# Kernel optimization log

Measured on AMD Instinct MI355X. Metric: run time of the kernel, lower is better.

The kernel has to match this reference:

```python
import jax, jax.numpy as jnp
import numpy as np

B, N, D = 8, 4096, 128
P, K = 256, 64            # n_patches, n_pts_per_patch (= FoldingNet num_fine)
DFF, GRID = 1024, 2
G2 = GRID * GRID
NC = K // G2              # num_coarse
EPS = 1e-5                # BatchNorm eps (eval mode, running stats)


def fps(xyz, n):
    """Farthest point sampling on one cloud xyz [N,3] -> n int32 indices."""
    Np = xyz.shape[0]
    def step(carry, _):
        mind, last = carry
        d = jnp.sum((xyz - xyz[last]) ** 2, -1)
        mind = jnp.minimum(mind, d)
        nxt = jnp.argmax(mind).astype(jnp.int32)
        return (mind, nxt), nxt
    (_, _), idx = jax.lax.scan(step, (jnp.full((Np,), 1e10, xyz.dtype), jnp.int32(0)), None, length=n - 1)
    return jnp.concatenate([jnp.zeros((1,), jnp.int32), idx])


def setup_inputs() -> dict:
    key = jax.random.key(0)
    ks = jax.random.split(key, 24)
    rn = lambda i, s, sc=1.0: sc * jax.random.normal(ks[i], s, dtype=jnp.float32)
    inp = {
        'xyz': rn(0, (B, N, 3)),
        'feat': rn(1, (B, N, D)),
        # FoldingNet.xyz_mlp (Linear weights stored [in,out])
        'w1': rn(2, (D, DFF), 0.09), 'b1': rn(3, (DFF,), 0.02),
        'w2': rn(4, (DFF, DFF), 0.03), 'b2': rn(5, (DFF,), 0.02),
        'w3': rn(6, (DFF, 3 * NC), 0.03), 'b3': rn(7, (3 * NC,), 0.02),
        # FoldingNet.final_conv (1x1 conv weights stored [in,out]), BN eval stats
        'cw1': rn(8, (D + 5, DFF), 0.09), 'cb1': rn(9, (DFF,), 0.02),
        'g1': 0.5 + jax.random.uniform(ks[10], (DFF,), dtype=jnp.float32),
        'be1': rn(11, (DFF,), 0.02), 'm1': rn(12, (DFF,), 0.1),
        'v1': 0.5 + jax.random.uniform(ks[13], (DFF,), dtype=jnp.float32),
        'cw2': rn(14, (DFF, DFF), 0.03), 'cb2': rn(15, (DFF,), 0.02),
        'g2': 0.5 + jax.random.uniform(ks[16], (DFF,), dtype=jnp.float32),
        'be2': rn(17, (DFF,), 0.02), 'm2': rn(18, (DFF,), 0.1),
        'v2': 0.5 + jax.random.uniform(ks[19], (DFF,), dtype=jnp.float32),
        'cw3': rn(20, (DFF, 3), 0.03), 'cb3': rn(21, (3,), 0.02),
    }
    return inp


def reference(xyz, feat, w1, b1, w2, b2, w3, b3,
              cw1, cb1, g1, be1, m1, v1,
              cw2, cb2, g2, be2, m2, v2, cw3, cb3):
    # ---- point_forward: FPS -> square_distance -> masked topk -> gather -> maxpool ----
    fidx = jax.vmap(lambda p: fps(p, P))(xyz)                          # [B,P]
    patch_xyz = jnp.take_along_axis(xyz, fidx[:, :, None], 1)          # [B,P,3]
    d = (jnp.sum(xyz ** 2, -1)[:, :, None]
         + jnp.sum(patch_xyz ** 2, -1)[:, None, :]
         - 2.0 * jnp.einsum('bnc,bpc->bnp', xyz, patch_xyz))           # [B,N,P]
    # equal-sized dense batches => to_dense_batch mask is all-true (no 1e10 fill needed)
    _, gidx = jax.lax.top_k(-jnp.swapaxes(d, 1, 2), K)                 # [B,P,K] nearest
    bidx = jnp.arange(B)[:, None, None]
    grouped_feat = feat[bidx, gidx]                                    # [B,P,K,D]
    patch_feat = jnp.max(grouped_feat, axis=-2)                        # [B,P,D]
    grouped_xyz_norm = xyz[bidx, gidx] - patch_xyz[:, :, None, :]      # [B,P,K,3]

    # ---- FoldingNet decoder ----
    pf = patch_feat.reshape(B * P, D)
    h = jax.nn.relu(pf @ w1 + b1)
    h = jax.nn.relu(h @ w2 + b2)
    coarse = (h @ w3 + b3).reshape(B * P, NC, 3)                       # [BP,NC,3]
    pts = jnp.repeat(coarse, G2, axis=1)                               # [BP,K,3] (center)
    a = jnp.linspace(-0.05, 0.05, GRID, dtype=pf.dtype)
    seed2 = jnp.stack([jnp.tile(a, GRID), jnp.repeat(a, GRID)], -1)    # [G2,2]
    seedf = jnp.tile(seed2, (NC, 1))                                   # [K,2]
    featc = jnp.concatenate([
        jnp.broadcast_to(pf[:, None, :], (B * P, K, D)),
        jnp.broadcast_to(seedf[None], (B * P, K, 2)),
        pts], axis=-1)                                                 # [BP,K,D+5]
    bn = lambda x, g, be, m, v: (x - m) * (g * jax.lax.rsqrt(v + EPS)) + be
    h1 = jax.nn.relu(bn(featc @ cw1 + cb1, g1, be1, m1, v1))
    h2 = jax.nn.relu(bn(h1 @ cw2 + cb2, g2, be2, m2, v2))
    fine = h2 @ cw3 + cb3 + pts                                        # [BP,K,3]

    # ---- Chamfer L2 (mean(dist1)+mean(dist2)) between fine and grouped points ----
    gxyz = grouped_xyz_norm.reshape(B * P, K, 3)
    dd = jnp.sum((fine[:, :, None, :] - gxyz[:, None, :, :]) ** 2, -1) # [BP,K,K]
    loss_recon = jnp.mean(jnp.min(dd, axis=2)) + jnp.mean(jnp.min(dd, axis=1))
    return loss_recon
```

## Files before the change

kernel.cpp:

```cpp
#include <hip/hip_runtime.h>
#include <hip/hip_bf16.h>
#include <stdint.h>

#define DEV __device__ __forceinline__

using bf16x8  = __attribute__((ext_vector_type(8))) __bf16;
using floatx4 = __attribute__((ext_vector_type(4))) float;
using int32x8 = __attribute__((ext_vector_type(8))) int;

constexpr int Bb  = 8;
constexpr int Nn  = 4096;
constexpr int Dd  = 128;
constexpr int Pp  = 256;
constexpr int Kk  = 64;
constexpr int BP  = Bb * Pp;
constexpr int M2  = BP * Kk;
constexpr float EPSBN = 1e-5f;

DEV unsigned short f2bf(float f) {
  uint32_t u = __float_as_uint(f);
  u += 0x7fffu + ((u >> 16) & 1u);
  return (unsigned short)(u >> 16);
}
DEV float bf2f(unsigned short h) { return __uint_as_float(((uint32_t)h) << 16); }

DEV void async_copy16(const void* g, const void* l) {
  __builtin_amdgcn_global_load_lds(
      (__attribute__((address_space(1))) uint32_t*)(uintptr_t)g,
      (__attribute__((address_space(3))) uint32_t*)(uint32_t)(uintptr_t)l,
      16, 0, 0);
}

__global__ void prep_k(const float* g1, const float* be1, const float* m1, const float* v1, const float* cb1,
                       const float* g2, const float* be2, const float* m2, const float* v2, const float* cb2,
                       float* sc1, float* sh1, float* sc2, float* sh2, float* out) {
  int t = threadIdx.x;
  float s1 = g1[t] * rsqrtf(v1[t] + EPSBN);
  sc1[t] = s1; sh1[t] = (cb1[t] - m1[t]) * s1 + be1[t];
  float s2 = g2[t] * rsqrtf(v2[t] + EPSBN);
  sc2[t] = s2; sh2[t] = (cb2[t] - m2[t]) * s2 + be2[t];
  if (t == 0) out[0] = 0.f;
}

__global__ void cvt16(const float* __restrict__ in, unsigned short* __restrict__ out, int Kd, int Nd) {
  __shared__ float ts[32][33];
  int tx = threadIdx.x & 31, ty = threadIdx.x >> 5;
  int n0 = blockIdx.x * 32, k0 = blockIdx.y * 32;
#pragma unroll
  for (int r = 0; r < 4; ++r)
    ts[ty + 8 * r][tx] = in[(size_t)(k0 + ty + 8 * r) * Nd + n0 + tx];
  __syncthreads();
#pragma unroll
  for (int r = 0; r < 4; ++r)
    out[(size_t)(n0 + ty + 8 * r) * Kd + k0 + tx] = f2bf(ts[tx][ty + 8 * r]);
}

__global__ void cvt8(const float* __restrict__ in, uint8_t* __restrict__ out, int Kd, int Nd) {
  __shared__ float ts[32][33];
  int tx = threadIdx.x & 31, ty = threadIdx.x >> 5;
  int n0 = blockIdx.x * 32, k0 = blockIdx.y * 32;
#pragma unroll
  for (int r = 0; r < 4; ++r)
    ts[ty + 8 * r][tx] = in[(size_t)(k0 + ty + 8 * r) * Nd + n0 + tx];
  __syncthreads();
#pragma unroll
  for (int r = 0; r < 4; ++r) {
    float v = ts[tx][ty + 8 * r];
    int w = __builtin_amdgcn_cvt_pk_fp8_f32(v, v, 0, false);
    out[(size_t)(n0 + ty + 8 * r) * Kd + k0 + tx] = (uint8_t)(w & 0xff);
  }
}

#define DPPF(v, CTRL) __uint_as_float((uint32_t)__builtin_amdgcn_update_dpp( \
    (int)__float_as_uint(v), (int)__float_as_uint(v), CTRL, 0xF, 0xF, false))
#define DPPI(v, CTRL) __builtin_amdgcn_update_dpp(v, v, CTRL, 0xF, 0xF, false)
#define RSTEP2(CTRL) { \
    float od = DPPF(bv, CTRL); \
    int oi = DPPI(bi, CTRL); \
    bool tk = (od > bv) || (od == bv && oi < bi); \
    bv = tk ? od : bv; bi = tk ? oi : bi; }

__global__ __launch_bounds__(256)
void fps_k(const float* __restrict__ xyz, float* __restrict__ pxyz) {
  int b = blockIdx.x, tid = threadIdx.x;
  int lane = tid & 63, wv = tid >> 6;
  __shared__ float xs[Nn], ys[Nn], zs[Nn];
  __shared__ uint64_t cand[2][4];
  float xr[16], yr[16], zr[16], md[16];
#pragma unroll
  for (int j = 0; j < 16; ++j) {
    int i = tid + j * 256;
    const float* q = &xyz[(size_t)(b * Nn + i) * 3];
    float x = q[0], y = q[1], z = q[2];
    xr[j] = x; yr[j] = y; zr[j] = z; md[j] = 1e10f;
    xs[i] = x; ys[i] = y; zs[i] = z;
  }
  __syncthreads();
  const float* q0 = &xyz[(size_t)(b * Nn) * 3];
  float lx = q0[0], ly = q0[1], lz = q0[2];
  if (tid == 0) {
    pxyz[(size_t)(b * Pp) * 3 + 0] = lx;
    pxyz[(size_t)(b * Pp) * 3 + 1] = ly;
    pxyz[(size_t)(b * Pp) * 3 + 2] = lz;
  }
  for (int p = 1; p < Pp; ++p) {
    float bv = -1.f; int bi = 0x7fffffff;
#pragma unroll
    for (int j = 0; j < 16; ++j) {
      float dx = __fadd_rn(xr[j], -lx);
      float dy = __fadd_rn(yr[j], -ly);
      float dz = __fadd_rn(zr[j], -lz);
      float d = __fadd_rn(__fadd_rn(__fmul_rn(dx, dx), __fmul_rn(dy, dy)), __fmul_rn(dz, dz));
      float m = fminf(md[j], d);
      md[j] = m;
      if (m > bv) { bv = m; bi = tid + j * 256; }
    }
    RSTEP2(0x111) RSTEP2(0x112) RSTEP2(0x114) RSTEP2(0x118) RSTEP2(0x142) RSTEP2(0x143)
    int s = p & 1;
    if (lane == 63)
      cand[s][wv] = ((uint64_t)(uint32_t)__float_as_uint(bv) << 32) |
                    (uint32_t)(0x7fffffff - bi);
    __syncthreads();
    uint64_t k0 = cand[s][0], k1 = cand[s][1], k2 = cand[s][2], k3 = cand[s][3];
    uint64_t ka = (k0 > k1) ? k0 : k1;
    uint64_t kb = (k2 > k3) ? k2 : k3;
    uint64_t kw = (ka > kb) ? ka : kb;
    int wi = 0x7fffffff - (int)(uint32_t)(kw & 0xffffffffu);
    lx = xs[wi]; ly = ys[wi]; lz = zs[wi];
    if (tid == 0) {
      pxyz[(size_t)(b * Pp + p) * 3 + 0] = lx;
      pxyz[(size_t)(b * Pp + p) * 3 + 1] = ly;
      pxyz[(size_t)(b * Pp + p) * 3 + 2] = lz;
    }
  }
}

__global__ __launch_bounds__(256)
void group_k(const float* __restrict__ xyz, const float* __restrict__ feat,
             const float* __restrict__ pxyz, unsigned short* __restrict__ pfb,
             float* __restrict__ gxyz) {
  int bp = blockIdx.x, tid = threadIdx.x;
  int b = bp >> 8;
  __shared__ uint32_t dbits[Nn];
  __shared__ uint32_t hist[256];
  __shared__ int sel[64];
  __shared__ uint32_t svDigit, svWant, svClt, svCeq;
  __shared__ float red[256];
  float px = pxyz[(size_t)bp * 3], py = pxyz[(size_t)bp * 3 + 1], pz = pxyz[(size_t)bp * 3 + 2];
  for (int i = tid; i < Nn; i += 256) {
    const float* q = &xyz[(size_t)(b * Nn + i) * 3];
    float dx = q[0] - px, dy = q[1] - py, dz = q[2] - pz;
    dbits[i] = __float_as_uint(dx * dx + dy * dy + dz * dz);
  }
  uint32_t prefix = 0, want = 64;
  for (int shift = 24; shift >= 0; shift -= 8) {
    __syncthreads();
    hist[tid] = 0;
    __syncthreads();
    for (int i = tid; i < Nn; i += 256) {
      uint32_t v = dbits[i];
      bool match = (shift == 24) || ((v >> (shift + 8)) == prefix);
      if (match) atomicAdd(&hist[(v >> shift) & 255], 1u);
    }
    __syncthreads();
    uint32_t myh = hist[tid];
    for (int off = 1; off < 256; off <<= 1) {
      uint32_t o = (tid >= off) ? hist[tid - off] : 0u;
      __syncthreads();
      hist[tid] += o;
      __syncthreads();
    }
    uint32_t cum = hist[tid];
    uint32_t prev = cum - myh;
    if (prev < want && want <= cum) { svDigit = (uint32_t)tid; svWant = want - prev; }
    __syncthreads();
    prefix = (prefix << 8) | svDigit;
    want = svWant;
  }
  uint32_t tval = prefix;
  if (tid == 0) { svClt = 0; svCeq = 0; }
  __syncthreads();
  for (int i = tid; i < Nn; i += 256) {
    if (dbits[i] < tval) { uint32_t pos = atomicAdd(&svClt, 1u); sel[pos] = i; }
  }
  __syncthreads();
  uint32_t clt = svClt;
  for (int i = tid; i < Nn; i += 256) {
    if (dbits[i] == tval) {
      uint32_t pos = atomicAdd(&svCeq, 1u);
      if (clt + pos < 64) sel[clt + pos] = i;
    }
  }
  __syncthreads();
  if (tid < 192) {
    int k = tid / 3, c = tid - k * 3;
    float sub = (c == 0) ? px : (c == 1) ? py : pz;
    gxyz[(size_t)bp * 192 + tid] = xyz[(size_t)(b * Nn + sel[k]) * 3 + c] - sub;
  }
  int dch = tid & 127, half = tid >> 7;
  float m = -1e30f;
  for (int k = half * 32; k < half * 32 + 32; ++k)
    m = fmaxf(m, feat[(size_t)(b * Nn + sel[k]) * Dd + dch]);
  red[tid] = m;
  __syncthreads();
  if (half == 0) pfb[(size_t)bp * Dd + dch] = f2bf(fmaxf(m, red[tid + 128]));
}

template <int EPI>
__global__ __launch_bounds__(256)
void gemm_bt(const unsigned short* __restrict__ A, const unsigned short* __restrict__ Bt,
             float* __restrict__ Cf, unsigned short* __restrict__ Ch,
             const float* __restrict__ p0,
             int Npar, int Kd, int nbn) {
  __shared__ __align__(16) unsigned short As[128 * 32];
  __shared__ __align__(16) unsigned short Bs[128 * 32];
  const int tid = threadIdx.x;
  const int lane = tid & 63, wid = tid >> 6;
  const int bn = blockIdx.x % nbn, bm = blockIdx.x / nbn;
  const int m0 = bm * 128, n0 = bn * 128;
  const int quad = lane >> 4, l15 = lane & 15;
  const int wm = wid & 1, wn = wid >> 1;

  floatx4 acc[4][4];
#pragma unroll
  for (int i = 0; i < 4; ++i)
#pragma unroll
    for (int j = 0; j < 4; ++j) acc[i][j] = floatx4{0.f, 0.f, 0.f, 0.f};

  const int c0i = tid, c1i = tid + 256;
  const int r0 = c0i >> 2, o0 = (c0i & 3) * 8;
  const int r1 = c1i >> 2, o1 = (c1i & 3) * 8;

  for (int k0 = 0; k0 < Kd; k0 += 32) {
    async_copy16(A + (size_t)(m0 + r0) * Kd + k0 + o0, &As[c0i * 8]);
    async_copy16(A + (size_t)(m0 + r1) * Kd + k0 + o1, &As[c1i * 8]);
    async_copy16(Bt + (size_t)(n0 + r0) * Kd + k0 + o0, &Bs[c0i * 8]);
    async_copy16(Bt + (size_t)(n0 + r1) * Kd + k0 + o1, &Bs[c1i * 8]);
    __syncthreads();
    const bf16x8* Ap = reinterpret_cast<const bf16x8*>(As);
    const bf16x8* Bp = reinterpret_cast<const bf16x8*>(Bs);
    bf16x8 af[4], bfv[4];
#pragma unroll
    for (int t = 0; t < 4; ++t) {
      af[t]  = Ap[(wm * 64 + t * 16 + l15) * 4 + quad];
      bfv[t] = Bp[(wn * 64 + t * 16 + l15) * 4 + quad];
    }
#pragma unroll
    for (int mt = 0; mt < 4; ++mt)
#pragma unroll
      for (int nt = 0; nt < 4; ++nt)
        acc[mt][nt] = __builtin_amdgcn_mfma_f32_16x16x32_bf16(af[mt], bfv[nt], acc[mt][nt], 0, 0, 0);
    __syncthreads();
  }

  const int rowBase = m0 + wm * 64 + quad * 4;
  const int colBase = n0 + wn * 64 + l15;

  if (EPI == 0) {
#pragma unroll
    for (int mt = 0; mt < 4; ++mt)
#pragma unroll
      for (int nt = 0; nt < 4; ++nt)
#pragma unroll
        for (int r = 0; r < 4; ++r)
          Cf[(size_t)(rowBase + mt * 16 + r) * Npar + colBase + nt * 16] = acc[mt][nt][r];
  } else {
#pragma unroll
    for (int nt = 0; nt < 4; ++nt) {
      float bias = p0[colBase + nt * 16];
#pragma unroll
      for (int mt = 0; mt < 4; ++mt)
#pragma unroll
        for (int r = 0; r < 4; ++r) {
          float v = fmaxf(acc[mt][nt][r] + bias, 0.f);
          Ch[(size_t)(rowBase + mt * 16 + r) * Npar + colBase + nt * 16] = f2bf(v);
        }
    }
  }
}

__global__ __launch_bounds__(256)
void gemm_mx3(const float* __restrict__ u1, const float* __restrict__ cw1,
              const float* __restrict__ coarse, const float* __restrict__ sc1,
              const float* __restrict__ sh1,
              const uint8_t* __restrict__ Bt,
              const float* __restrict__ p0, const float* __restrict__ p1,
              const float* __restrict__ cw3, const float* __restrict__ cb3,
              float* __restrict__ fine) {
  __shared__ __align__(128) uint8_t As[32 * 1024];
  __shared__ __align__(128) uint8_t Bs[128 * 128];
  __shared__ float fsum[2][2][16][3];
  const int tid = threadIdx.x;
  const int lane = tid & 63, wid = tid >> 6;
  const int bm = blockIdx.x;
  const int quad = lane >> 4, l15 = lane & 15;
  const int wm = wid & 1, wn = wid >> 1;
  const int bp = bm >> 1;

  {
    int n0c = tid * 4;
    float4 un  = *(const float4*)&u1[(size_t)bp * 1024 + n0c];
    float4 a0  = *(const float4*)&cw1[128 * 1024 + n0c];
    float4 a1  = *(const float4*)&cw1[129 * 1024 + n0c];
    float4 b0  = *(const float4*)&cw1[130 * 1024 + n0c];
    float4 b1v = *(const float4*)&cw1[131 * 1024 + n0c];
    float4 b2v = *(const float4*)&cw1[132 * 1024 + n0c];
    float4 sc  = *(const float4*)&sc1[n0c];
    float4 sh  = *(const float4*)&sh1[n0c];
    const float sxv[4] = {-0.05f, 0.05f, -0.05f, 0.05f};
    const float syv[4] = {-0.05f, -0.05f, 0.05f, 0.05f};
    uint32_t* Aw = (uint32_t*)As;
    int gc = tid >> 2;
    int dw = tid & 3;
    for (int row = 0; row < 32; ++row) {
      int gi = row & 3;
      int j = (bm & 1) * 8 + (row >> 2);
      float c0 = coarse[(size_t)bp * 48 + j * 3 + 0];
      float c1 = coarse[(size_t)bp * 48 + j * 3 + 1];
      float c2 = coarse[(size_t)bp * 48 + j * 3 + 2];
      float sx = sxv[gi], sy = syv[gi];
      float x0 = un.x + sx * a0.x + sy * a1.x + c0 * b0.x + c1 * b1v.x + c2 * b2v.x;
      float x1 = un.y + sx * a0.y + sy * a1.y + c0 * b0.y + c1 * b1v.y + c2 * b2v.y;
      float x2 = un.z + sx * a0.z + sy * a1.z + c0 * b0.z + c1 * b1v.z + c2 * b2v.z;
      float x3 = un.w + sx * a0.w + sy * a1.w + c0 * b0.w + c1 * b1v.w + c2 * b2v.w;
      float v0 = fmaxf(x0 * sc.x + sh.x, 0.f);
      float v1 = fmaxf(x1 * sc.y + sh.y, 0.f);
      float v2 = fmaxf(x2 * sc.z + sh.z, 0.f);
      float v3 = fmaxf(x3 * sc.w + sh.w, 0.f);
      int w = __builtin_amdgcn_cvt_pk_fp8_f32(v0, v1, 0, false);
      w = __builtin_amdgcn_cvt_pk_fp8_f32(v2, v3, w, true);
      int phys = (gc & ~7) | ((gc & 7) ^ (row & 7));
      Aw[row * 256 + phys * 4 + dw] = (uint32_t)w;
    }
  }
  float fp[4][3];
#pragma unroll
  for (int r = 0; r < 4; ++r) fp[r][0] = fp[r][1] = fp[r][2] = 0.f;
  __syncthreads();

  const uint4* Ap = (const uint4*)As;
  const int rm = wm * 16 + l15;
  const int swm = rm & 7;

  for (int bn = 0; bn < 8; ++bn) {
    const int n0 = bn * 128;
    floatx4 acc[4];
#pragma unroll
    for (int j = 0; j < 4; ++j) acc[j] = floatx4{0.f, 0.f, 0.f, 0.f};

    for (int k0 = 0; k0 < 1024; k0 += 128) {
#pragma unroll
      for (int c = 0; c < 4; ++c) {
        int ci = c * 256 + tid;
        int row = ci >> 3, cp = ci & 7;
        int cc = cp ^ (row & 7);
        async_copy16(Bt + (size_t)(n0 + row) * 1024 + k0 + cc * 16, &Bs[ci * 16]);
      }
      __syncthreads();
      const uint4* Bp = (const uint4*)Bs;
      int kc = k0 >> 4;
      uint4 alo = Ap[rm * 64 + kc + ((2 * quad) ^ swm)];
      uint4 ahi = Ap[rm * 64 + kc + ((2 * quad + 1) ^ swm)];
      int32x8 av = int32x8{(int)alo.x, (int)alo.y, (int)alo.z, (int)alo.w,
                           (int)ahi.x, (int)ahi.y, (int)ahi.z, (int)ahi.w};
      int32x8 bv[4];
#pragma unroll
      for (int nt = 0; nt < 4; ++nt) {
        int rn = wn * 64 + nt * 16 + l15;
        int swn = rn & 7;
        uint4 blo = Bp[rn * 8 + ((2 * quad) ^ swn)];
        uint4 bhi = Bp[rn * 8 + ((2 * quad + 1) ^ swn)];
        bv[nt] = int32x8{(int)blo.x, (int)blo.y, (int)blo.z, (int)blo.w,
                         (int)bhi.x, (int)bhi.y, (int)bhi.z, (int)bhi.w};
      }
#pragma unroll
      for (int nt = 0; nt < 4; ++nt)
        acc[nt] = __builtin_amdgcn_mfma_scale_f32_16x16x128_f8f6f4(
            av, bv[nt], acc[nt], 0, 0, 0, 127, 0, 127);
      __syncthreads();
    }

#pragma unroll
    for (int nt = 0; nt < 4; ++nt) {
      int col = n0 + wn * 64 + nt * 16 + l15;
      float sc = p0[col], sh = p1[col];
      float c0 = cw3[col * 3], c1 = cw3[col * 3 + 1], c2 = cw3[col * 3 + 2];
#pragma unroll
      for (int r = 0; r < 4; ++r) {
        float v = fmaxf(acc[nt][r] * sc + sh, 0.f);
        fp[r][0] += v * c0; fp[r][1] += v * c1; fp[r][2] += v * c2;
      }
    }
  }

#pragma unroll
  for (int off = 1; off < 16; off <<= 1)
#pragma unroll
    for (int r = 0; r < 4; ++r)
#pragma unroll
      for (int i = 0; i < 3; ++i)
        fp[r][i] += __shfl_xor(fp[r][i], off, 64);
  if (l15 == 0) {
#pragma unroll
    for (int r = 0; r < 4; ++r)
#pragma unroll
      for (int i = 0; i < 3; ++i)
        fsum[wm][wn][quad * 4 + r][i] = fp[r][i];
  }
  __syncthreads();
  if (tid < 96) {
    int row = tid / 3, i = tid - row * 3;
    float s = fsum[row >> 4][0][row & 15][i] + fsum[row >> 4][1][row & 15][i];
    int g = bm * 32 + row;
    int j = (bm & 1) * 8 + ((row & 31) >> 2);
    fine[(size_t)g * 3 + i] = s + cb3[i] + coarse[(size_t)bp * 48 + j * 3 + i];
  }
}

__global__ __launch_bounds__(256)
void coarse_k(const unsigned short* __restrict__ h2m, const float* __restrict__ w3,
              const float* __restrict__ b3, float* __restrict__ coarse) {
  int r = blockIdx.x, tid = threadIdx.x;
  __shared__ float hrow[1024];
  __shared__ float part[192];
  for (int i = tid; i < 1024; i += 256) hrow[i] = bf2f(h2m[(size_t)r * 1024 + i]);
  __syncthreads();
  if (tid < 192) {
    int j = tid % 48, seg = tid / 48;
    float acc = 0.f;
    for (int k = seg * 256; k < seg * 256 + 256; ++k) acc += hrow[k] * w3[(size_t)k * 48 + j];
    part[tid] = acc;
  }
  __syncthreads();
  if (tid < 48)
    coarse[(size_t)r * 48 + tid] = part[tid] + part[tid + 48] + part[tid + 96] + part[tid + 144] + b3[tid];
}

__global__ __launch_bounds__(256)
void chamfer_k(const float* __restrict__ fine, const float* __restrict__ gxyz,
               float* __restrict__ out) {
  int tid = threadIdx.x, wv = tid >> 6, lane = tid & 63;
  int bp = blockIdx.x * 4 + wv;
  __shared__ float sf[4][64][3], sg[4][64][3];
  const float* fr = &fine[(size_t)(bp * 64 + lane) * 3];
  const float* gr = &gxyz[(size_t)(bp * 64 + lane) * 3];
  sf[wv][lane][0] = fr[0]; sf[wv][lane][1] = fr[1]; sf[wv][lane][2] = fr[2];
  sg[wv][lane][0] = gr[0]; sg[wv][lane][1] = gr[1]; sg[wv][lane][2] = gr[2];
  __syncthreads();
  float f0 = sf[wv][lane][0], f1 = sf[wv][lane][1], f2 = sf[wv][lane][2];
  float g0 = sg[wv][lane][0], g1 = sg[wv][lane][1], g2 = sg[wv][lane][2];
  float rmin = 1e30f, cmin = 1e30f;
  for (int j = 0; j < 64; ++j) {
    float dx = f0 - sg[wv][j][0], dy = f1 - sg[wv][j][1], dz = f2 - sg[wv][j][2];
    rmin = fminf(rmin, dx * dx + dy * dy + dz * dz);
    float ex = sf[wv][j][0] - g0, ey = sf[wv][j][1] - g1, ez = sf[wv][j][2] - g2;
    cmin = fminf(cmin, ex * ex + ey * ey + ez * ez);
  }
  float tot = rmin + cmin;
  for (int off = 32; off; off >>= 1) tot += __shfl_down(tot, off, 64);
  if (lane == 0) atomicAdd(out, tot * (1.0f / 131072.0f));
}

extern "C" void kernel_launch(void* const* d_in, const int* in_sizes, int n_in,
                              void* d_out, int out_size, void* d_ws, size_t ws_size,
                              hipStream_t stream) {
  (void)in_sizes; (void)n_in; (void)out_size; (void)ws_size;
  const float* xyz = (const float*)d_in[0];
  const float* feat = (const float*)d_in[1];
  const float* w1 = (const float*)d_in[2];
  const float* b1 = (const float*)d_in[3];
  const float* w2 = (const float*)d_in[4];
  const float* b2 = (const float*)d_in[5];
  const float* w3 = (const float*)d_in[6];
  const float* b3 = (const float*)d_in[7];
  const float* cw1 = (const float*)d_in[8];
  const float* cb1 = (const float*)d_in[9];
  const float* g1 = (const float*)d_in[10];
  const float* be1 = (const float*)d_in[11];
  const float* m1 = (const float*)d_in[12];
  const float* v1 = (const float*)d_in[13];
  const float* cw2 = (const float*)d_in[14];
  const float* cb2 = (const float*)d_in[15];
  const float* g2 = (const float*)d_in[16];
  const float* be2 = (const float*)d_in[17];
  const float* m2 = (const float*)d_in[18];
  const float* v2 = (const float*)d_in[19];
  const float* cw3 = (const float*)d_in[20];
  const float* cb3 = (const float*)d_in[21];
  float* out = (float*)d_out;

  uint8_t* ws = (uint8_t*)d_ws;
  size_t off = 0;
  auto alloc = [&](size_t bytes) {
    void* p = ws + off;
    off = (off + bytes + 255) & ~(size_t)255;
    return p;
  };
  float*          pxyz  = (float*)alloc((size_t)BP * 3 * 4);
  unsigned short* w1t   = (unsigned short*)alloc((size_t)1024 * 128 * 2);
  unsigned short* cw1t  = (unsigned short*)alloc((size_t)1024 * 128 * 2);
  unsigned short* w2t   = (unsigned short*)alloc((size_t)1024 * 1024 * 2);
  uint8_t*        cw2t8 = (uint8_t*)alloc((size_t)1024 * 1024);
  float*          sc1   = (float*)alloc(4096);
  float*          sh1   = (float*)alloc(4096);
  float*          sc2   = (float*)alloc(4096);
  float*          sh2   = (float*)alloc(4096);
  unsigned short* pfb   = (unsigned short*)alloc((size_t)BP * 128 * 2);
  float*          gxyz  = (float*)alloc((size_t)BP * 64 * 3 * 4);
  float*          u1    = (float*)alloc((size_t)BP * 1024 * 4);
  unsigned short* hb    = (unsigned short*)alloc((size_t)BP * 1024 * 2);
  unsigned short* h2m   = (unsigned short*)alloc((size_t)BP * 1024 * 2);
  float*          coarse = (float*)alloc((size_t)BP * 48 * 4);
  float*          fine  = (float*)alloc((size_t)M2 * 3 * 4);

  prep_k<<<1, 1024, 0, stream>>>(g1, be1, m1, v1, cb1, g2, be2, m2, v2, cb2,
                                 sc1, sh1, sc2, sh2, out);
  cvt16<<<dim3(1024 / 32, 128 / 32), 256, 0, stream>>>(w1, w1t, 128, 1024);
  cvt16<<<dim3(1024 / 32, 128 / 32), 256, 0, stream>>>(cw1, cw1t, 128, 1024);
  cvt16<<<dim3(1024 / 32, 1024 / 32), 256, 0, stream>>>(w2, w2t, 1024, 1024);
  cvt8<<<dim3(1024 / 32, 1024 / 32), 256, 0, stream>>>(cw2, cw2t8, 1024, 1024);
  fps_k<<<Bb, 256, 0, stream>>>(xyz, pxyz);
  group_k<<<BP, 256, 0, stream>>>(xyz, feat, pxyz, pfb, gxyz);
  gemm_bt<0><<<(2048 / 128) * 8, 256, 0, stream>>>(pfb, cw1t, u1, nullptr, nullptr,
                                                   1024, 128, 8);
  gemm_bt<1><<<(2048 / 128) * 8, 256, 0, stream>>>(pfb, w1t, nullptr, hb, b1,
                                                   1024, 128, 8);
  gemm_bt<1><<<(2048 / 128) * 8, 256, 0, stream>>>(hb, w2t, nullptr, h2m, b2,
                                                   1024, 1024, 8);
  coarse_k<<<2048, 256, 0, stream>>>(h2m, w3, b3, coarse);
  gemm_mx3<<<M2 / 32, 256, 0, stream>>>(u1, cw1, coarse, sc1, sh1,
                                        cw2t8, sc2, sh2, cw3, cb3, fine);
  chamfer_k<<<BP / 4, 256, 0, stream>>>(fine, gxyz, out);
}
```

Baseline: 691.0 us.

## Enlarge fused MX-FP8 GEMM tile to 128 rows with double-buffered B staging

```diff
diff --git a/kernel.cpp b/kernel.cpp
--- a/kernel.cpp
+++ b/kernel.cpp
@@ -279,7 +279,7 @@
   }
 }
 
-__global__ __launch_bounds__(256)
+__global__ __launch_bounds__(256, 1)
 void gemm_mx3(const float* __restrict__ u1, const float* __restrict__ cw1,
               const float* __restrict__ coarse, const float* __restrict__ sc1,
               const float* __restrict__ sh1,
@@ -287,19 +287,35 @@
               const float* __restrict__ p0, const float* __restrict__ p1,
               const float* __restrict__ cw3, const float* __restrict__ cb3,
               float* __restrict__ fine) {
-  __shared__ __align__(128) uint8_t As[32 * 1024];
-  __shared__ __align__(128) uint8_t Bs[128 * 128];
-  __shared__ float fsum[2][2][16][3];
+  __shared__ __align__(128) uint8_t As[128 * 1024];
+  __shared__ __align__(128) uint8_t Bs[2][128 * 128];
   const int tid = threadIdx.x;
   const int lane = tid & 63, wid = tid >> 6;
   const int bm = blockIdx.x;
   const int quad = lane >> 4, l15 = lane & 15;
   const int wm = wid & 1, wn = wid >> 1;
-  const int bp = bm >> 1;
+  const int bp0 = bm * 2;
+
+  auto stageB = [&](int it, uint8_t* buf) {
+    int n0 = (it >> 3) * 128, k0 = (it & 7) * 128;
+#pragma unroll
+    for (int c = 0; c < 4; ++c) {
+      int ci = c * 256 + tid;
+      int row = ci >> 3, cp = ci & 7;
+      int cc = cp ^ (row & 7);
+      async_copy16(Bt + (size_t)(n0 + row) * 1024 + k0 + cc * 16, &buf[ci * 16]);
+    }
+  };
+
+  stageB(0, Bs[0]);
+  float* coLds = (float*)Bs[1];
+  if (tid < 96) coLds[tid] = coarse[(size_t)bp0 * 48 + tid];
+  __syncthreads();
 
   {
     int n0c = tid * 4;
-    float4 un  = *(const float4*)&u1[(size_t)bp * 1024 + n0c];
+    float4 un0 = *(const float4*)&u1[(size_t)bp0 * 1024 + n0c];
+    float4 un1 = *(const float4*)&u1[(size_t)(bp0 + 1) * 1024 + n0c];
     float4 a0  = *(const float4*)&cw1[128 * 1024 + n0c];
     float4 a1  = *(const float4*)&cw1[129 * 1024 + n0c];
     float4 b0  = *(const float4*)&cw1[130 * 1024 + n0c];
@@ -310,19 +326,26 @@
     const float sxv[4] = {-0.05f, 0.05f, -0.05f, 0.05f};
     const float syv[4] = {-0.05f, -0.05f, 0.05f, 0.05f};
     uint32_t* Aw = (uint32_t*)As;
-    int gc = tid >> 2;
-    int dw = tid & 3;
-    for (int row = 0; row < 32; ++row) {
-      int gi = row & 3;
-      int j = (bm & 1) * 8 + (row >> 2);
-      float c0 = coarse[(size_t)bp * 48 + j * 3 + 0];
-      float c1 = coarse[(size_t)bp * 48 + j * 3 + 1];
-      float c2 = coarse[(size_t)bp * 48 + j * 3 + 2];
-      float sx = sxv[gi], sy = syv[gi];
-      float x0 = un.x + sx * a0.x + sy * a1.x + c0 * b0.x + c1 * b1v.x + c2 * b2v.x;
-      float x1 = un.y + sx * a0.y + sy * a1.y + c0 * b0.y + c1 * b1v.y + c2 * b2v.y;
-      float x2 = un.z + sx * a0.z + sy * a1.z + c0 * b0.z + c1 * b1v.z + c2 * b2v.z;
-      float x3 = un.w + sx * a0.w + sy * a1.w + c0 * b0.w + c1 * b1v.w + c2 * b2v.w;
+    int gc = tid >> 2, dw = tid & 3;
+    float t0 = 0.f, t1 = 0.f, t2 = 0.f, t3 = 0.f;
+    for (int row = 0; row < 128; ++row) {
+      int h = row >> 6;
+      if ((row & 3) == 0) {
+        int j = (row & 63) >> 2;
+        float c0 = coLds[h * 48 + j * 3 + 0];
+        float c1 = coLds[h * 48 + j * 3 + 1];
+        float c2 = coLds[h * 48 + j * 3 + 2];
+        t0 = c0 * b0.x + c1 * b1v.x + c2 * b2v.x;
+        t1 = c0 * b0.y + c1 * b1v.y + c2 * b2v.y;
+        t2 = c0 * b0.z + c1 * b1v.z + c2 * b2v.z;
+        t3 = c0 * b0.w + c1 * b1v.w + c2 * b2v.w;
+      }
+      float sx = sxv[row & 3], sy = syv[row & 3];
+      float4 un = h ? un1 : un0;
+      float x0 = un.x + sx * a0.x + sy * a1.x + t0;
+      float x1 = un.y + sx * a0.y + sy * a1.y + t1;
+      float x2 = un.z + sx * a0.z + sy * a1.z + t2;
+      float x3 = un.w + sx * a0.w + sy * a1.w + t3;
       float v0 = fmaxf(x0 * sc.x + sh.x, 0.f);
       float v1 = fmaxf(x1 * sc.y + sh.y, 0.f);
       float v2 = fmaxf(x2 * sc.z + sh.z, 0.f);
@@ -333,86 +356,97 @@
       Aw[row * 256 + phys * 4 + dw] = (uint32_t)w;
     }
   }
-  float fp[4][3];
-#pragma unroll
-  for (int r = 0; r < 4; ++r) fp[r][0] = fp[r][1] = fp[r][2] = 0.f;
-  __syncthreads();
+  float fp[4][4][3];
+#pragma unroll
+  for (int mt = 0; mt < 4; ++mt)
+#pragma unroll
+    for (int r = 0; r < 4; ++r)
+      fp[mt][r][0] = fp[mt][r][1] = fp[mt][r][2] = 0.f;
 
   const uint4* Ap = (const uint4*)As;
-  const int rm = wm * 16 + l15;
-  const int swm = rm & 7;
-
+  int it = 0;
   for (int bn = 0; bn < 8; ++bn) {
-    const int n0 = bn * 128;
-    floatx4 acc[4];
-#pragma unroll
-    for (int j = 0; j < 4; ++j) acc[j] = floatx4{0.f, 0.f, 0.f, 0.f};
-
-    for (int k0 = 0; k0 < 1024; k0 += 128) {
-#pragma unroll
-      for (int c = 0; c < 4; ++c) {
-        int ci = c * 256 + tid;
-        int row = ci >> 3, cp = ci & 7;
-        int cc = cp ^ (row & 7);
-        async_copy16(Bt + (size_t)(n0 + row) * 1024 + k0 + cc * 16, &Bs[ci * 16]);
-      }
+    floatx4 acc[4][4];
+#pragma unroll
+    for (int i = 0; i < 4; ++i)
+#pragma unroll
+      for (int j = 0; j < 4; ++j) acc[i][j] = floatx4{0.f, 0.f, 0.f, 0.f};
+
+    for (int k0i = 0; k0i < 8; ++k0i) {
       __syncthreads();
-      const uint4* Bp = (const uint4*)Bs;
-      int kc = k0 >> 4;
-      uint4 alo = Ap[rm * 64 + kc + ((2 * quad) ^ swm)];
-      uint4 ahi = Ap[rm * 64 + kc + ((2 * quad + 1) ^ swm)];
-      int32x8 av = int32x8{(int)alo.x, (int)alo.y, (int)alo.z, (int)alo.w,
-                           (int)ahi.x, (int)ahi.y, (int)ahi.z, (int)ahi.w};
-      int32x8 bv[4];
-#pragma unroll
-      for (int nt = 0; nt < 4; ++nt) {
-        int rn = wn * 64 + nt * 16 + l15;
+      if (it + 1 < 64) stageB(it + 1, Bs[(it + 1) & 1]);
+      const uint4* Bp = (const uint4*)Bs[it & 1];
+      int kc = k0i * 8;
+      int32x8 av[4], bv[4];
+#pragma unroll
+      for (int t = 0; t < 4; ++t) {
+        int rm = wm * 64 + t * 16 + l15;
+        int swm = rm & 7;
+        uint4 alo = Ap[rm * 64 + kc + ((2 * quad) ^ swm)];
+        uint4 ahi = Ap[rm * 64 + kc + ((2 * quad + 1) ^ swm)];
+        int rn = wn * 64 + t * 16 + l15;
         int swn = rn & 7;
         uint4 blo = Bp[rn * 8 + ((2 * quad) ^ swn)];
         uint4 bhi = Bp[rn * 8 + ((2 * quad + 1) ^ swn)];
-        bv[nt] = int32x8{(int)blo.x, (int)blo.y, (int)blo.z, (int)blo.w,
-                         (int)bhi.x, (int)bhi.y, (int)bhi.z, (int)bhi.w};
+        av[t] = int32x8{(int)alo.x, (int)alo.y, (int)alo.z, (int)alo.w,
+                        (int)ahi.x, (int)ahi.y, (int)ahi.z, (int)ahi.w};
+        bv[t] = int32x8{(int)blo.x, (int)blo.y, (int)blo.z, (int)blo.w,
+                        (int)bhi.x, (int)bhi.y, (int)bhi.z, (int)bhi.w};
       }
 #pragma unroll
-      for (int nt = 0; nt < 4; ++nt)
-        acc[nt] = __builtin_amdgcn_mfma_scale_f32_16x16x128_f8f6f4(
-            av, bv[nt], acc[nt], 0, 0, 0, 127, 0, 127);
-      __syncthreads();
-    }
-
+      for (int mt = 0; mt < 4; ++mt)
+#pragma unroll
+        for (int nt = 0; nt < 4; ++nt)
+          acc[mt][nt] = __builtin_amdgcn_mfma_scale_f32_16x16x128_f8f6f4(
+              av[mt], bv[nt], acc[mt][nt], 0, 0, 0, 127, 0, 127);
+      ++it;
+    }
+
+    const int n0 = bn * 128;
 #pragma unroll
     for (int nt = 0; nt < 4; ++nt) {
       int col = n0 + wn * 64 + nt * 16 + l15;
       float sc = p0[col], sh = p1[col];
       float c0 = cw3[col * 3], c1 = cw3[col * 3 + 1], c2 = cw3[col * 3 + 2];
 #pragma unroll
+      for (int mt = 0; mt < 4; ++mt)
+#pragma unroll
+        for (int r = 0; r < 4; ++r) {
+          float v = fmaxf(acc[mt][nt][r] * sc + sh, 0.f);
+          fp[mt][r][0] += v * c0; fp[mt][r][1] += v * c1; fp[mt][r][2] += v * c2;
+        }
+    }
+  }
+
+#pragma unroll
+  for (int off = 1; off < 16; off <<= 1)
+#pragma unroll
+    for (int mt = 0; mt < 4; ++mt)
+#pragma unroll
+      for (int r = 0; r < 4; ++r)
+#pragma unroll
+        for (int i = 0; i < 3; ++i)
+          fp[mt][r][i] += __shfl_xor(fp[mt][r][i], off, 64);
+  __syncthreads();
+  float* fs = (float*)Bs[0];
+  if (l15 == 0) {
+#pragma unroll
+    for (int mt = 0; mt < 4; ++mt)
+#pragma unroll
       for (int r = 0; r < 4; ++r) {
-        float v = fmaxf(acc[nt][r] * sc + sh, 0.f);
-        fp[r][0] += v * c0; fp[r][1] += v * c1; fp[r][2] += v * c2;
+        int rowLocal = mt * 16 + quad * 4 + r;
+#pragma unroll
+        for (int i = 0; i < 3; ++i)
+          fs[((wm * 2 + wn) * 64 + rowLocal) * 3 + i] = fp[mt][r][i];
       }
-    }
-  }
-
-#pragma unroll
-  for (int off = 1; off < 16; off <<= 1)
-#pragma unroll
-    for (int r = 0; r < 4; ++r)
-#pragma unroll
-      for (int i = 0; i < 3; ++i)
-        fp[r][i] += __shfl_xor(fp[r][i], off, 64);
-  if (l15 == 0) {
-#pragma unroll
-    for (int r = 0; r < 4; ++r)
-#pragma unroll
-      for (int i = 0; i < 3; ++i)
-        fsum[wm][wn][quad * 4 + r][i] = fp[r][i];
-  }
-  __syncthreads();
-  if (tid < 96) {
-    int row = tid / 3, i = tid - row * 3;
-    float s = fsum[row >> 4][0][row & 15][i] + fsum[row >> 4][1][row & 15][i];
-    int g = bm * 32 + row;
-    int j = (bm & 1) * 8 + ((row & 31) >> 2);
+  }
+  __syncthreads();
+  for (int t = tid; t < 128 * 3; t += 256) {
+    int row = t / 3, i = t - row * 3;
+    int h = row >> 6, rl = row & 63;
+    float s = fs[((h * 2 + 0) * 64 + rl) * 3 + i] + fs[((h * 2 + 1) * 64 + rl) * 3 + i];
+    int g = bm * 128 + row;
+    int bp = bp0 + h, j = rl >> 2;
     fine[(size_t)g * 3 + i] = s + cb3[i] + coarse[(size_t)bp * 48 + j * 3 + i];
   }
 }
@@ -528,7 +562,7 @@
   gemm_bt<1><<<(2048 / 128) * 8, 256, 0, stream>>>(hb, w2t, nullptr, h2m, b2,
                                                    1024, 1024, 8);
   coarse_k<<<2048, 256, 0, stream>>>(h2m, w3, b3, coarse);
-  gemm_mx3<<<M2 / 32, 256, 0, stream>>>(u1, cw1, coarse, sc1, sh1,
-                                        cw2t8, sc2, sh2, cw3, cb3, fine);
+  gemm_mx3<<<M2 / 128, 256, 0, stream>>>(u1, cw1, coarse, sc1, sh1,
+                                         cw2t8, sc2, sh2, cw3, cb3, fine);
   chamfer_k<<<BP / 4, 256, 0, stream>>>(fine, gxyz, out);
 }
```

After: 868.3 us. 1.26x slower.
